# Optimization experiments

Hardware: AMD Instinct MI355X
Metric: run time of the kernel (lower is better)

## Reference

```python
import jax, jax.numpy as jnp
import numpy as np

B, C, L, D = 8, 32, 2048, 128
R, H = 8, 4  # num_routers, num_heads


def setup_inputs() -> dict:
    key = jax.random.key(0)
    ks = jax.random.split(key, 20)
    p = lambda k, shape: jax.random.normal(k, shape, dtype=jnp.float32) * 0.02
    inp = {
        "Z": jax.random.normal(ks[0], (B, C, L, D), dtype=jnp.float32),
        "router": p(ks[1], (R, D)),
        # router_sender projections (d_model -> d_model, torch Linear stored as x@W+b)
        "Wq1": p(ks[2], (D, D)), "bq1": jnp.zeros((D,), jnp.float32),
        "Wk1": p(ks[3], (D, D)), "bk1": jnp.zeros((D,), jnp.float32),
        "Wv1": p(ks[4], (D, D)), "bv1": jnp.zeros((D,), jnp.float32),
        "Wo1": p(ks[5], (D, D)), "bo1": jnp.zeros((D,), jnp.float32),
        # router_receiver projections
        "Wq2": p(ks[6], (D, D)), "bq2": jnp.zeros((D,), jnp.float32),
        "Wk2": p(ks[7], (D, D)), "bk2": jnp.zeros((D,), jnp.float32),
        "Wv2": p(ks[8], (D, D)), "bv2": jnp.zeros((D,), jnp.float32),
        "Wo2": p(ks[9], (D, D)), "bo2": jnp.zeros((D,), jnp.float32),
        # LayerNorm
        "gamma": jnp.ones((D,), jnp.float32),
        "beta": jnp.zeros((D,), jnp.float32),
    }
    return inp


def _cross_attn(q_in, k_in, v_in, Wq, bq, Wk, bk, Wv, bv, Wo, bo):
    # Informer FullAttention + AttentionLayer (dropout=0)
    Bn, Lq, Dm = q_in.shape
    Lk = k_in.shape[1]
    dh = Dm // H
    q = (q_in @ Wq + bq).reshape(Bn, Lq, H, dh)
    k = (k_in @ Wk + bk).reshape(Bn, Lk, H, dh)
    v = (v_in @ Wv + bv).reshape(Bn, Lk, H, dh)
    scale = 1.0 / np.sqrt(dh)
    scores = jnp.einsum("blhe,bshe->bhls", q, k) * scale
    A = jax.nn.softmax(scores, axis=-1)
    out = jnp.einsum("bhls,bshd->blhd", A, v).reshape(Bn, Lq, Dm)
    return out @ Wo + bo


def _layernorm(x, gamma, beta, eps=1e-5):
    mu = jnp.mean(x, axis=-1, keepdims=True)
    var = jnp.mean(jnp.square(x - mu), axis=-1, keepdims=True)
    return (x - mu) * jax.lax.rsqrt(var + eps) * gamma + beta


def reference(Z, router, Wq1, bq1, Wk1, bk1, Wv1, bv1, Wo1, bo1,
              Wq2, bq2, Wk2, bk2, Wv2, bv2, Wo2, bo2, gamma, beta):
    Bz, Cz, Lz, Dz = Z.shape
    x = Z.reshape(Bz * Cz, Lz, Dz)
    batch_router = jnp.broadcast_to(router[None], (Bz * Cz, R, Dz))
    # stage 1: routers attend to the sequence (R x L)
    router_buffer = _cross_attn(batch_router, x, x,
                                Wq1, bq1, Wk1, bk1, Wv1, bv1, Wo1, bo1)
    # stage 2: sequence attends to routers (L x R)
    router_receive = _cross_attn(x, router_buffer, router_buffer,
                                 Wq2, bq2, Wk2, bk2, Wv2, bv2, Wo2, bo2)
    out = _layernorm(x + router_receive, gamma, beta)
    return out.reshape(Bz, Cz, Lz, Dz)
```

## Files before the change

### kernel.cpp

```cpp
#include <hip/hip_runtime.h>

typedef float f4_t __attribute__((ext_vector_type(4)));
typedef __bf16 bf8_t __attribute__((ext_vector_type(8)));
typedef __bf16 bf4_t __attribute__((ext_vector_type(4)));

#define MFMA16(a,b,c) __builtin_amdgcn_mfma_f32_16x16x32_bf16((a),(b),(c),0,0,0)

static constexpr float kScale = 0.17677669529663687f;

__global__ __launch_bounds__(256) void k0_fold(
    const float* __restrict__ router, const float* __restrict__ Wq1,
    const float* __restrict__ bq1, const float* __restrict__ Wk1,
    const float* __restrict__ bk1, __bf16* __restrict__ q1t,
    float* __restrict__ c1)
{
  __shared__ float q1[8][128];
  const int t = threadIdx.x;
  for (int idx = t; idx < 1024; idx += 256) {
    int r = idx >> 7, dp = idx & 127;
    float acc = bq1[dp];
    for (int e = 0; e < 128; ++e) acc += router[r*128 + e] * Wq1[e*128 + dp];
    q1[r][dp] = acc;
  }
  __syncthreads();
  for (int idx = t; idx < 4096; idx += 256) {
    int j = idx >> 7, e = idx & 127;
    int h = j >> 3, r = j & 7;
    float acc = 0.f;
    for (int d = 0; d < 32; ++d) acc += q1[r][h*32 + d] * Wk1[e*128 + h*32 + d];
    q1t[idx] = (__bf16)(acc * kScale);
  }
  if (t < 32) {
    int h = t >> 3, r = t & 7;
    float acc = 0.f;
    for (int d = 0; d < 32; ++d) acc += q1[r][h*32 + d] * bk1[h*32 + d];
    c1[t] = acc * kScale;
  }
}

__global__ __launch_bounds__(512) void k1_stage1(
    const float* __restrict__ Z, const __bf16* __restrict__ q1t_g,
    const float* __restrict__ c1_g, float* __restrict__ xap,
    float* __restrict__ lp, __bf16* __restrict__ xws)
{
  __shared__ __bf16 xb[64][136];
  __shared__ __bf16 xT[128][72];
  __shared__ __bf16 PT[32][72];
  __shared__ float lds_l[32];

  const int tid = threadIdx.x;
  const int bid = blockIdx.x;
  const float* xbase = Z + (size_t)bid * (256 * 128);
  __bf16* xwb = xws + (size_t)bid * (256 * 128);

  if (tid < 32) lds_l[tid] = 0.f;

  const int lane = tid & 63;
  const int w = tid >> 6;
  const int lc = lane & 15;
  const int lg = lane >> 4;
  const int ms = w >> 2;
  const int ns = w & 3;
  float c1v[4];
#pragma unroll
  for (int r2 = 0; r2 < 4; ++r2) c1v[r2] = c1_g[ms*16 + lg*4 + r2];
  bf8_t aq[4];
#pragma unroll
  for (int ks = 0; ks < 4; ++ks)
    aq[ks] = *(const bf8_t*)(q1t_g + (ms*16 + lc)*128 + ks*32 + lg*8);

  const f4_t fzero = {0.f, 0.f, 0.f, 0.f};
  f4_t accxa[2] = { fzero, fzero };
  float Lacc[4] = {0.f, 0.f, 0.f, 0.f};

  const int spos = tid >> 5;
  const int sd0  = (tid & 31) << 2;

  f4_t zr[4];
#pragma unroll
  for (int i = 0; i < 4; ++i)
    zr[i] = __builtin_nontemporal_load(
        (const f4_t*)(xbase + (spos + i*16)*128 + sd0));

  __syncthreads();

  for (int tile = 0; tile < 4; ++tile) {
#pragma unroll
    for (int i = 0; i < 4; ++i) {
      int pos = spos + i*16;
      bf4_t b4 = { (__bf16)zr[i].x, (__bf16)zr[i].y, (__bf16)zr[i].z, (__bf16)zr[i].w };
      *(bf4_t*)&xb[pos][sd0] = b4;
      *(bf4_t*)(xwb + (tile*64 + pos)*128 + sd0) = b4;
    }
    __syncthreads();

    if (tile < 3) {
      const float* xt = xbase + (tile + 1) * (64 * 128);
#pragma unroll
      for (int i = 0; i < 4; ++i)
        zr[i] = __builtin_nontemporal_load(
            (const f4_t*)(xt + (spos + i*16)*128 + sd0));
    }

#pragma unroll
    for (int s = 0; s < 2; ++s) {
      int u = tid + s*512;
      int dim = u & 127, pb = (u >> 7) << 3;
      bf8_t t8;
#pragma unroll
      for (int p = 0; p < 8; ++p) t8[p] = xb[pb + p][dim];
      *(bf8_t*)&xT[dim][pb] = t8;
    }
    f4_t sacc = fzero;
#pragma unroll
    for (int ks = 0; ks < 4; ++ks) {
      bf8_t b = *(const bf8_t*)&xb[ns*16 + lc][ks*32 + lg*8];
      sacc = MFMA16(aq[ks], b, sacc);
    }
    const int posn = ns*16 + lc;
#pragma unroll
    for (int r2 = 0; r2 < 4; ++r2) {
      float p = __expf(sacc[r2] + c1v[r2]);
      Lacc[r2] += p;
      PT[ms*16 + lg*4 + r2][posn] = (__bf16)p;
    }
    __syncthreads();

#pragma unroll
    for (int nt = 0; nt < 2; ++nt) {
      const int dimt = (ns << 1) + nt;
#pragma unroll
      for (int ks = 0; ks < 2; ++ks) {
        bf8_t a = *(const bf8_t*)&PT[ms*16 + lc][ks*32 + lg*8];
        bf8_t b = *(const bf8_t*)&xT[dimt*16 + lc][ks*32 + lg*8];
        accxa[nt] = MFMA16(a, b, accxa[nt]);
      }
    }
    __syncthreads();
  }

#pragma unroll
  for (int r2 = 0; r2 < 4; ++r2) {
    float v = Lacc[r2];
    v += __shfl_xor(v, 1);
    v += __shfl_xor(v, 2);
    v += __shfl_xor(v, 4);
    v += __shfl_xor(v, 8);
    if (lc == 0) atomicAdd(&lds_l[ms*16 + lg*4 + r2], v);
  }
  __syncthreads();

  float* xo = xap + (size_t)bid * 4096;
#pragma unroll
  for (int nt = 0; nt < 2; ++nt) {
    const int dim = ((ns << 1) + nt)*16 + lc;
#pragma unroll
    for (int r2 = 0; r2 < 4; ++r2) {
      int j = ms*16 + lg*4 + r2;
      xo[j*128 + dim] = accxa[nt][r2];
    }
  }
  if (tid < 32) lp[bid*32 + tid] = lds_l[tid];
}

__global__ __launch_bounds__(256) void k1b_mid(
    const float* __restrict__ xap, const float* __restrict__ lp,
    const float* __restrict__ Wv1, const float* __restrict__ bv1,
    const float* __restrict__ Wo1, const float* __restrict__ bo1,
    const float* __restrict__ Wk2, const float* __restrict__ bk2,
    const float* __restrict__ Wv2, const float* __restrict__ bv2,
    const float* __restrict__ Wq2, const float* __restrict__ bq2,
    const float* __restrict__ Wo2,
    __bf16* __restrict__ kt2, float* __restrict__ c2, __bf16* __restrict__ vt2)
{
  __shared__ float xa[32][129];
  __shared__ float invl[32];
  __shared__ float out1[8][128];
  __shared__ float rb[8][128];
  __shared__ float k2s[8][128];
  __shared__ float v2s[8][128];

  const int t = threadIdx.x, b = blockIdx.x;
  for (int idx = t; idx < 4096; idx += 256) {
    float s = 0.f;
#pragma unroll
    for (int k = 0; k < 8; ++k)
      s += xap[(size_t)(b*8 + k) * 4096 + idx];
    xa[idx >> 7][idx & 127] = s;
  }
  if (t < 32) {
    float s = 0.f;
#pragma unroll
    for (int k = 0; k < 8; ++k) s += lp[(b*8 + k)*32 + t];
    invl[t] = 1.f / s;
  }
  __syncthreads();

  for (int idx = t; idx < 1024; idx += 256) {
    int r = idx >> 7, hd = idx & 127, h = hd >> 5;
    int j = h*8 + r;
    float acc = 0.f;
    for (int e = 0; e < 128; ++e) acc += xa[j][e] * Wv1[e*128 + hd];
    out1[r][hd] = acc * invl[j] + bv1[hd];
  }
  __syncthreads();
  for (int idx = t; idx < 1024; idx += 256) {
    int r = idx >> 7, e2 = idx & 127;
    float acc = bo1[e2];
    for (int hd = 0; hd < 128; ++hd) acc += out1[r][hd] * Wo1[hd*128 + e2];
    rb[r][e2] = acc;
  }
  __syncthreads();
  for (int idx = t; idx < 2048; idx += 256) {
    int sel = idx >> 10;
    int r = (idx >> 7) & 7, hd = idx & 127;
    const float* W = sel ? Wv2 : Wk2;
    const float* bb = sel ? bv2 : bk2;
    float acc = bb[hd];
    for (int e = 0; e < 128; ++e) acc += rb[r][e] * W[e*128 + hd];
    float (*dst)[128] = sel ? v2s : k2s;
    dst[r][hd] = acc;
  }
  __syncthreads();
  for (int idx = t; idx < 4096; idx += 256) {
    int j = idx >> 7, e = idx & 127;
    int h = j >> 3, r = j & 7;
    float acck = 0.f, accv = 0.f;
    for (int d = 0; d < 32; ++d) {
      acck += Wq2[e*128 + h*32 + d] * k2s[r][h*32 + d];
      accv += v2s[r][h*32 + d] * Wo2[(h*32 + d)*128 + e];
    }
    kt2[(size_t)b*4096 + j*128 + e] = (__bf16)(acck * kScale);
    vt2[(size_t)b*4096 + e*32 + j] = (__bf16)accv;
  }
  if (t < 32) {
    int h = t >> 3, r = t & 7;
    float acc = 0.f;
    for (int d = 0; d < 32; ++d) acc += bq2[h*32 + d] * k2s[r][h*32 + d];
    c2[b*32 + t] = acc * kScale;
  }
}

__global__ __launch_bounds__(512) void k2_stage2(
    const __bf16* __restrict__ xws, const __bf16* __restrict__ kt2,
    const float* __restrict__ c2g, const __bf16* __restrict__ vt2,
    const float* __restrict__ bo2, const float* __restrict__ gamma,
    const float* __restrict__ beta, float* __restrict__ out)
{
  __shared__ __bf16 xb[128][136];
  __shared__ __bf16 P2[128][40];

  const int tid = threadIdx.x;
  const int bid = blockIdx.x;
  const int batch = bid >> 4;
  const __bf16* xsrc = xws + (size_t)bid * (128 * 128);
  float* y = out + (size_t)bid * (128 * 128);

  const __bf16* ktb = kt2 + (size_t)batch * 4096;
  const __bf16* vtb = vt2 + (size_t)batch * 4096;

  const int lane = tid & 63;
  const int w = tid >> 6;
  const int lc = lane & 15;
  const int lg = lane >> 4;

  float c2v[2] = { c2g[batch*32 + lc], c2g[batch*32 + 16 + lc] };

#pragma unroll
  for (int j = 0; j < 4; ++j) {
    int c = lane + j*64;
    int pos = w*16 + (c >> 4);
    int d0 = (c & 15) << 3;
    *(uint4*)&xb[pos][d0] = *(const uint4*)(xsrc + pos*128 + d0);
  }

  const f4_t fzero = {0.f, 0.f, 0.f, 0.f};

  f4_t sacc[2] = { fzero, fzero };
#pragma unroll
  for (int ks = 0; ks < 4; ++ks) {
    bf8_t a = *(const bf8_t*)&xb[w*16 + lc][ks*32 + lg*8];
#pragma unroll
    for (int nt = 0; nt < 2; ++nt) {
      bf8_t b = *(const bf8_t*)(ktb + (nt*16 + lc)*128 + ks*32 + lg*8);
      sacc[nt] = MFMA16(a, b, sacc[nt]);
    }
  }
#pragma unroll
  for (int nt = 0; nt < 2; ++nt) {
#pragma unroll
    for (int r2 = 0; r2 < 4; ++r2) {
      float p = __expf(sacc[nt][r2] + c2v[nt]);
      float sum = p;
      sum += __shfl_xor(sum, 1);
      sum += __shfl_xor(sum, 2);
      sum += __shfl_xor(sum, 4);
      P2[w*16 + lg*4 + r2][nt*16 + lc] = (__bf16)(p * __builtin_amdgcn_rcpf(sum));
    }
  }

  bf8_t pa = *(const bf8_t*)&P2[w*16 + lc][lg*8];
  f4_t racc[8];
#pragma unroll
  for (int nt = 0; nt < 8; ++nt) {
    bf8_t b = *(const bf8_t*)(vtb + (nt*16 + lc)*32 + lg*8);
    racc[nt] = MFMA16(pa, b, fzero);
  }

  float bo2v[8], gv[8], bv[8];
#pragma unroll
  for (int nt = 0; nt < 8; ++nt) {
    int dd = nt*16 + lc;
    bo2v[nt] = bo2[dd]; gv[nt] = gamma[dd]; bv[nt] = beta[dd];
  }
#pragma unroll
  for (int r2 = 0; r2 < 4; ++r2) {
    int pos = w*16 + lg*4 + r2;
    float vv[8];
    float s1 = 0.f, s2 = 0.f;
#pragma unroll
    for (int nt = 0; nt < 8; ++nt) {
      float xv = (float)xb[pos][nt*16 + lc];
      float tv = racc[nt][r2] + bo2v[nt] + xv;
      vv[nt] = tv; s1 += tv; s2 += tv*tv;
    }
    s1 += __shfl_xor(s1, 1); s1 += __shfl_xor(s1, 2);
    s1 += __shfl_xor(s1, 4); s1 += __shfl_xor(s1, 8);
    s2 += __shfl_xor(s2, 1); s2 += __shfl_xor(s2, 2);
    s2 += __shfl_xor(s2, 4); s2 += __shfl_xor(s2, 8);
    float mean = s1 * (1.f/128.f);
    float var = s2 * (1.f/128.f) - mean*mean;
    float rstd = rsqrtf(var + 1e-5f);
#pragma unroll
    for (int nt = 0; nt < 8; ++nt)
      __builtin_nontemporal_store((vv[nt] - mean) * rstd * gv[nt] + bv[nt],
                                  &y[pos*128 + nt*16 + lc]);
  }
}

extern "C" void kernel_launch(void* const* d_in, const int* in_sizes, int n_in,
                              void* d_out, int out_size, void* d_ws, size_t ws_size,
                              hipStream_t stream)
{
  const float* Z     = (const float*)d_in[0];
  const float* router= (const float*)d_in[1];
  const float* Wq1   = (const float*)d_in[2];
  const float* bq1   = (const float*)d_in[3];
  const float* Wk1   = (const float*)d_in[4];
  const float* bk1   = (const float*)d_in[5];
  const float* Wv1   = (const float*)d_in[6];
  const float* bv1   = (const float*)d_in[7];
  const float* Wo1   = (const float*)d_in[8];
  const float* bo1   = (const float*)d_in[9];
  const float* Wq2   = (const float*)d_in[10];
  const float* bq2   = (const float*)d_in[11];
  const float* Wk2   = (const float*)d_in[12];
  const float* bk2   = (const float*)d_in[13];
  const float* Wv2   = (const float*)d_in[14];
  const float* bv2   = (const float*)d_in[15];
  const float* Wo2   = (const float*)d_in[16];
  const float* bo2   = (const float*)d_in[17];
  const float* gamma = (const float*)d_in[18];
  const float* beta  = (const float*)d_in[19];
  float* out = (float*)d_out;

  char* base = (char*)d_ws;
  __bf16* q1tb = (__bf16*)(base);
  float*  c1   = (float*)(base + 8192);
  float*  c2   = (float*)(base + 16384);
  float*  lp   = (float*)(base + 65536);
  float*  xap  = (float*)(base + (1u<<20));
  __bf16* kt2b = (__bf16*)(base + (36u<<20));
  __bf16* vt2b = (__bf16*)(base + (38u<<20));
  __bf16* xws  = (__bf16*)(base + (40u<<20));
  (void)in_sizes; (void)n_in; (void)out_size; (void)ws_size;

  k0_fold<<<dim3(1), dim3(256), 0, stream>>>(router, Wq1, bq1, Wk1, bk1, q1tb, c1);
  k1_stage1<<<dim3(2048), dim3(512), 0, stream>>>(Z, q1tb, c1, xap, lp, xws);
  k1b_mid<<<dim3(256), dim3(256), 0, stream>>>(xap, lp, Wv1, bv1, Wo1, bo1,
                                               Wk2, bk2, Wv2, bv2, Wq2, bq2, Wo2,
                                               kt2b, c2, vt2b);
  k2_stage2<<<dim3(4096), dim3(512), 0, stream>>>(xws, kt2b, c2, vt2b, bo2, gamma, beta, out);
}
```

Before: 288.6 us.

## Make stage-2 persistent with register prefetch, widen stage-1 loads, parallelize fold

The stage-2 kernel becomes persistent: 512 blocks each walk 8 consecutive 128-row chunks and prefetch the next chunk's bf16 tile into registers while computing the current one. This amortizes per-block setup and overlaps loads with compute, but it cuts the number of resident waves per CU. Stage 1 now loads 8 floats per thread per row, stores 16-byte bf16 vectors, and drops a trailing per-tile barrier. The fold kernel is spread over 16 blocks instead of one.

```diff
diff --git a/kernel.cpp b/kernel.cpp
--- a/kernel.cpp
+++ b/kernel.cpp
@@ -15,7 +15,7 @@
     float* __restrict__ c1)
 {
   __shared__ float q1[8][128];
-  const int t = threadIdx.x;
+  const int t = threadIdx.x, b = blockIdx.x;
   for (int idx = t; idx < 1024; idx += 256) {
     int r = idx >> 7, dp = idx & 127;
     float acc = bq1[dp];
@@ -23,14 +23,15 @@
     q1[r][dp] = acc;
   }
   __syncthreads();
-  for (int idx = t; idx < 4096; idx += 256) {
+  {
+    int idx = b*256 + t;
     int j = idx >> 7, e = idx & 127;
     int h = j >> 3, r = j & 7;
     float acc = 0.f;
     for (int d = 0; d < 32; ++d) acc += q1[r][h*32 + d] * Wk1[e*128 + h*32 + d];
     q1t[idx] = (__bf16)(acc * kScale);
   }
-  if (t < 32) {
+  if (b == 0 && t < 32) {
     int h = t >> 3, r = t & 7;
     float acc = 0.f;
     for (int d = 0; d < 32; ++d) acc += q1[r][h*32 + d] * bk1[h*32 + d];
@@ -73,33 +74,39 @@
   f4_t accxa[2] = { fzero, fzero };
   float Lacc[4] = {0.f, 0.f, 0.f, 0.f};
 
-  const int spos = tid >> 5;
-  const int sd0  = (tid & 31) << 2;
+  const int srow = tid >> 4;
+  const int sd0  = (tid & 15) << 3;
 
   f4_t zr[4];
 #pragma unroll
-  for (int i = 0; i < 4; ++i)
-    zr[i] = __builtin_nontemporal_load(
-        (const f4_t*)(xbase + (spos + i*16)*128 + sd0));
+  for (int i = 0; i < 2; ++i) {
+    const float* p = xbase + (srow + 32*i)*128 + sd0;
+    zr[i*2]   = __builtin_nontemporal_load((const f4_t*)p);
+    zr[i*2+1] = __builtin_nontemporal_load((const f4_t*)(p + 4));
+  }
 
   __syncthreads();
 
   for (int tile = 0; tile < 4; ++tile) {
 #pragma unroll
-    for (int i = 0; i < 4; ++i) {
-      int pos = spos + i*16;
-      bf4_t b4 = { (__bf16)zr[i].x, (__bf16)zr[i].y, (__bf16)zr[i].z, (__bf16)zr[i].w };
-      *(bf4_t*)&xb[pos][sd0] = b4;
-      *(bf4_t*)(xwb + (tile*64 + pos)*128 + sd0) = b4;
+    for (int i = 0; i < 2; ++i) {
+      int pos = srow + 32*i;
+      f4_t v0 = zr[i*2], v1 = zr[i*2+1];
+      bf8_t b8 = { (__bf16)v0.x, (__bf16)v0.y, (__bf16)v0.z, (__bf16)v0.w,
+                   (__bf16)v1.x, (__bf16)v1.y, (__bf16)v1.z, (__bf16)v1.w };
+      *(bf8_t*)&xb[pos][sd0] = b8;
+      *(bf8_t*)(xwb + (tile*64 + pos)*128 + sd0) = b8;
     }
     __syncthreads();
 
     if (tile < 3) {
       const float* xt = xbase + (tile + 1) * (64 * 128);
 #pragma unroll
-      for (int i = 0; i < 4; ++i)
-        zr[i] = __builtin_nontemporal_load(
-            (const f4_t*)(xt + (spos + i*16)*128 + sd0));
+      for (int i = 0; i < 2; ++i) {
+        const float* p = xt + (srow + 32*i)*128 + sd0;
+        zr[i*2]   = __builtin_nontemporal_load((const f4_t*)p);
+        zr[i*2+1] = __builtin_nontemporal_load((const f4_t*)(p + 4));
+      }
     }
 
 #pragma unroll
@@ -136,7 +143,6 @@
         accxa[nt] = MFMA16(a, b, accxa[nt]);
       }
     }
-    __syncthreads();
   }
 
 #pragma unroll
@@ -251,10 +257,8 @@
   __shared__ __bf16 P2[128][40];
 
   const int tid = threadIdx.x;
-  const int bid = blockIdx.x;
-  const int batch = bid >> 4;
-  const __bf16* xsrc = xws + (size_t)bid * (128 * 128);
-  float* y = out + (size_t)bid * (128 * 128);
+  const int blk = blockIdx.x;
+  const int batch = blk >> 1;
 
   const __bf16* ktb = kt2 + (size_t)batch * 4096;
   const __bf16* vtb = vt2 + (size_t)batch * 4096;
@@ -265,76 +269,95 @@
   const int lg = lane >> 4;
 
   float c2v[2] = { c2g[batch*32 + lc], c2g[batch*32 + 16 + lc] };
-
-#pragma unroll
-  for (int j = 0; j < 4; ++j) {
-    int c = lane + j*64;
-    int pos = w*16 + (c >> 4);
-    int d0 = (c & 15) << 3;
-    *(uint4*)&xb[pos][d0] = *(const uint4*)(xsrc + pos*128 + d0);
-  }
-
-  const f4_t fzero = {0.f, 0.f, 0.f, 0.f};
-
-  f4_t sacc[2] = { fzero, fzero };
-#pragma unroll
-  for (int ks = 0; ks < 4; ++ks) {
-    bf8_t a = *(const bf8_t*)&xb[w*16 + lc][ks*32 + lg*8];
-#pragma unroll
-    for (int nt = 0; nt < 2; ++nt) {
-      bf8_t b = *(const bf8_t*)(ktb + (nt*16 + lc)*128 + ks*32 + lg*8);
-      sacc[nt] = MFMA16(a, b, sacc[nt]);
-    }
-  }
-#pragma unroll
-  for (int nt = 0; nt < 2; ++nt) {
-#pragma unroll
-    for (int r2 = 0; r2 < 4; ++r2) {
-      float p = __expf(sacc[nt][r2] + c2v[nt]);
-      float sum = p;
-      sum += __shfl_xor(sum, 1);
-      sum += __shfl_xor(sum, 2);
-      sum += __shfl_xor(sum, 4);
-      P2[w*16 + lg*4 + r2][nt*16 + lc] = (__bf16)(p * __builtin_amdgcn_rcpf(sum));
-    }
-  }
-
-  bf8_t pa = *(const bf8_t*)&P2[w*16 + lc][lg*8];
-  f4_t racc[8];
-#pragma unroll
-  for (int nt = 0; nt < 8; ++nt) {
-    bf8_t b = *(const bf8_t*)(vtb + (nt*16 + lc)*32 + lg*8);
-    racc[nt] = MFMA16(pa, b, fzero);
-  }
-
   float bo2v[8], gv[8], bv[8];
 #pragma unroll
   for (int nt = 0; nt < 8; ++nt) {
     int dd = nt*16 + lc;
     bo2v[nt] = bo2[dd]; gv[nt] = gamma[dd]; bv[nt] = beta[dd];
   }
-#pragma unroll
-  for (int r2 = 0; r2 < 4; ++r2) {
-    int pos = w*16 + lg*4 + r2;
-    float vv[8];
-    float s1 = 0.f, s2 = 0.f;
+
+  int spos[4], sd[4];
+#pragma unroll
+  for (int j = 0; j < 4; ++j) {
+    int c = lane + j*64;
+    spos[j] = w*16 + (c >> 4);
+    sd[j]   = (c & 15) << 3;
+  }
+
+  const size_t base0 = (size_t)blk * 8 * 16384;
+  uint4 zx[4];
+#pragma unroll
+  for (int j = 0; j < 4; ++j)
+    zx[j] = *(const uint4*)(xws + base0 + spos[j]*128 + sd[j]);
+
+  const f4_t fzero = {0.f, 0.f, 0.f, 0.f};
+
+  for (int c = 0; c < 8; ++c) {
+    const size_t cb = base0 + (size_t)c * 16384;
+#pragma unroll
+    for (int j = 0; j < 4; ++j)
+      *(uint4*)&xb[spos[j]][sd[j]] = zx[j];
+    if (c < 7) {
+#pragma unroll
+      for (int j = 0; j < 4; ++j)
+        zx[j] = *(const uint4*)(xws + cb + 16384 + spos[j]*128 + sd[j]);
+    }
+
+    f4_t sacc[2] = { fzero, fzero };
+#pragma unroll
+    for (int ks = 0; ks < 4; ++ks) {
+      bf8_t a = *(const bf8_t*)&xb[w*16 + lc][ks*32 + lg*8];
+#pragma unroll
+      for (int nt = 0; nt < 2; ++nt) {
+        bf8_t b = *(const bf8_t*)(ktb + (nt*16 + lc)*128 + ks*32 + lg*8);
+        sacc[nt] = MFMA16(a, b, sacc[nt]);
+      }
+    }
+#pragma unroll
+    for (int nt = 0; nt < 2; ++nt) {
+#pragma unroll
+      for (int r2 = 0; r2 < 4; ++r2) {
+        float p = __expf(sacc[nt][r2] + c2v[nt]);
+        float sum = p;
+        sum += __shfl_xor(sum, 1);
+        sum += __shfl_xor(sum, 2);
+        sum += __shfl_xor(sum, 4);
+        P2[w*16 + lg*4 + r2][nt*16 + lc] = (__bf16)(p * __builtin_amdgcn_rcpf(sum));
+      }
+    }
+
+    bf8_t pa = *(const bf8_t*)&P2[w*16 + lc][lg*8];
+    f4_t racc[8];
 #pragma unroll
     for (int nt = 0; nt < 8; ++nt) {
-      float xv = (float)xb[pos][nt*16 + lc];
-      float tv = racc[nt][r2] + bo2v[nt] + xv;
-      vv[nt] = tv; s1 += tv; s2 += tv*tv;
-    }
-    s1 += __shfl_xor(s1, 1); s1 += __shfl_xor(s1, 2);
-    s1 += __shfl_xor(s1, 4); s1 += __shfl_xor(s1, 8);
-    s2 += __shfl_xor(s2, 1); s2 += __shfl_xor(s2, 2);
-    s2 += __shfl_xor(s2, 4); s2 += __shfl_xor(s2, 8);
-    float mean = s1 * (1.f/128.f);
-    float var = s2 * (1.f/128.f) - mean*mean;
-    float rstd = rsqrtf(var + 1e-5f);
-#pragma unroll
-    for (int nt = 0; nt < 8; ++nt)
-      __builtin_nontemporal_store((vv[nt] - mean) * rstd * gv[nt] + bv[nt],
-                                  &y[pos*128 + nt*16 + lc]);
+      bf8_t b = *(const bf8_t*)(vtb + (nt*16 + lc)*32 + lg*8);
+      racc[nt] = MFMA16(pa, b, fzero);
+    }
+
+    float* y = out + cb;
+#pragma unroll
+    for (int r2 = 0; r2 < 4; ++r2) {
+      int pos = w*16 + lg*4 + r2;
+      float vv[8];
+      float s1 = 0.f, s2 = 0.f;
+#pragma unroll
+      for (int nt = 0; nt < 8; ++nt) {
+        float xv = (float)xb[pos][nt*16 + lc];
+        float tv = racc[nt][r2] + bo2v[nt] + xv;
+        vv[nt] = tv; s1 += tv; s2 += tv*tv;
+      }
+      s1 += __shfl_xor(s1, 1); s1 += __shfl_xor(s1, 2);
+      s1 += __shfl_xor(s1, 4); s1 += __shfl_xor(s1, 8);
+      s2 += __shfl_xor(s2, 1); s2 += __shfl_xor(s2, 2);
+      s2 += __shfl_xor(s2, 4); s2 += __shfl_xor(s2, 8);
+      float mean = s1 * (1.f/128.f);
+      float var = s2 * (1.f/128.f) - mean*mean;
+      float rstd = rsqrtf(var + 1e-5f);
+#pragma unroll
+      for (int nt = 0; nt < 8; ++nt)
+        __builtin_nontemporal_store((vv[nt] - mean) * rstd * gv[nt] + bv[nt],
+                                    &y[pos*128 + nt*16 + lc]);
+    }
   }
 }
 
@@ -375,10 +398,10 @@
   __bf16* xws  = (__bf16*)(base + (40u<<20));
   (void)in_sizes; (void)n_in; (void)out_size; (void)ws_size;
 
-  k0_fold<<<dim3(1), dim3(256), 0, stream>>>(router, Wq1, bq1, Wk1, bk1, q1tb, c1);
+  k0_fold<<<dim3(16), dim3(256), 0, stream>>>(router, Wq1, bq1, Wk1, bk1, q1tb, c1);
   k1_stage1<<<dim3(2048), dim3(512), 0, stream>>>(Z, q1tb, c1, xap, lp, xws);
   k1b_mid<<<dim3(256), dim3(256), 0, stream>>>(xap, lp, Wv1, bv1, Wo1, bo1,
                                                Wk2, bk2, Wv2, bv2, Wq2, bq2, Wo2,
                                                kt2b, c2, vt2b);
-  k2_stage2<<<dim3(4096), dim3(512), 0, stream>>>(xws, kt2b, c2, vt2b, bo2, gamma, beta, out);
+  k2_stage2<<<dim3(512), dim3(512), 0, stream>>>(xws, kt2b, c2, vt2b, bo2, gamma, beta, out);
 }
```

Measured after the change: 290.1 us. About the same (+0.5%).
